# Performance work log

Measured on AMD Instinct MI355X. Metric: run time of the kernel, lower is better.

## Reference

```python
import jax, jax.numpy as jnp
import numpy as np

N_HEAD = 16
N_EMBED = 1024

def setup_inputs() -> dict:
    key = jax.random.key(0)
    ks = jax.random.split(key, 5)
    C = N_EMBED
    x = jax.random.normal(ks[0], (2, 2048, C), dtype=jnp.float32)
    # c_attn: Linear(C, 3C); c_proj: Linear(C, C). PyTorch Linear: y = x @ W.T + b
    w_attn = jax.random.normal(ks[1], (3 * C, C), dtype=jnp.float32) * (1.0 / np.sqrt(C))
    b_attn = jnp.zeros((3 * C,), dtype=jnp.float32)
    w_proj = jax.random.normal(ks[2], (C, C), dtype=jnp.float32) * (1.0 / np.sqrt(C))
    b_proj = jnp.zeros((C,), dtype=jnp.float32)
    return {"x": x, "w_attn": w_attn, "b_attn": b_attn, "w_proj": w_proj, "b_proj": b_proj}

def reference(x, w_attn, b_attn, w_proj, b_proj):
    B, T, C = x.shape
    H = N_HEAD
    D = C // H
    qkv = jnp.einsum('btc,fc->btf', x, w_attn) + b_attn  # [B,T,3C]
    q, k, v = jnp.split(qkv, 3, axis=-1)
    # [B,H,T,D]
    q = q.reshape(B, T, H, D).transpose(0, 2, 1, 3)
    k = k.reshape(B, T, H, D).transpose(0, 2, 1, 3)
    v = v.reshape(B, T, H, D).transpose(0, 2, 1, 3)
    att = jnp.einsum('bhqd,bhkd->bhqk', q, k) * (1.0 / np.sqrt(D))  # [B,H,T,T]
    causal = jnp.tril(jnp.ones((T, T), dtype=bool))
    att = jnp.where(causal[None, None], att, jnp.finfo(att.dtype).min)
    att = jax.nn.softmax(att, axis=-1)
    y = jnp.einsum('bhqk,bhkd->bhqd', att, v)  # [B,H,T,D]
    y = y.transpose(0, 2, 1, 3).reshape(B, T, C)
    return jnp.einsum('btc,fc->btf', y, w_proj) + b_proj
```

## Files before the change

kernel.cpp:

```cpp
#include <hip/hip_runtime.h>
#include <hip/hip_bf16.h>

typedef unsigned short u16;
typedef __attribute__((ext_vector_type(8))) short v8s;
typedef __attribute__((ext_vector_type(4))) short v4s;
typedef __attribute__((ext_vector_type(4))) float v4f;

__device__ __forceinline__ u16 f2bu(float f) {
  union { float f; unsigned u; } v; v.f = f;
  unsigned r = (v.u + 0x7fffu + ((v.u >> 16) & 1u)) >> 16;
  return (u16)r;
}
__device__ __forceinline__ v4s pack4(const v4f& a) {
  union { v4s s; __hip_bfloat162 h[2]; } u;
  u.h[0] = __float22bfloat162_rn(make_float2(a[0], a[1]));
  u.h[1] = __float22bfloat162_rn(make_float2(a[2], a[3]));
  return u.s;
}
__device__ __forceinline__ v8s pack8(const v4f& a, const v4f& b) {
  union { v8s s; __hip_bfloat162 h[4]; } u;
  u.h[0] = __float22bfloat162_rn(make_float2(a[0], a[1]));
  u.h[1] = __float22bfloat162_rn(make_float2(a[2], a[3]));
  u.h[2] = __float22bfloat162_rn(make_float2(b[0], b[1]));
  u.h[3] = __float22bfloat162_rn(make_float2(b[2], b[3]));
  return u.s;
}

__device__ __forceinline__ void g2l16(const u16* g, u16* l) {
  __builtin_amdgcn_global_load_lds((const __attribute__((address_space(1))) void*)g,
                                   (__attribute__((address_space(3))) void*)l,
                                   16, 0, 0);
}

__global__ __launch_bounds__(256) void cvt_bf16(const float* __restrict__ s0, u16* __restrict__ d0, int n0,
                                                const float* __restrict__ s1, u16* __restrict__ d1, int n1,
                                                const float* __restrict__ s2, u16* __restrict__ d2, int n2) {
  int total8 = (n0 + n1 + n2) >> 3;
  for (int i = blockIdx.x * blockDim.x + threadIdx.x; i < total8; i += gridDim.x * blockDim.x) {
    int e = i << 3;
    const float* s; u16* d;
    if (e < n0)            { s = s0 + e;            d = d0 + e; }
    else if (e < n0 + n1)  { s = s1 + (e - n0);     d = d1 + (e - n0); }
    else                   { s = s2 + (e - n0 - n1); d = d2 + (e - n0 - n1); }
    v4f a = *(const v4f*)s, b = *(const v4f*)(s + 4);
    *(v8s*)d = pack8(a, b);
  }
}

__global__ __launch_bounds__(256) void gemm_qkv(const u16* __restrict__ A,
                                                const u16* __restrict__ W,
                                                const float* __restrict__ bias,
                                                u16* __restrict__ o0,
                                                u16* __restrict__ o1,
                                                u16* __restrict__ o2) {
  constexpr int K = 1024;
  __shared__ __align__(16) u16 As[128 * 64];
  __shared__ __align__(16) u16 Bs[128 * 64];
  const int tid = threadIdx.x;
  const int w = tid >> 6, lane = tid & 63, l15 = lane & 15, quad = lane >> 4;
  const int wm = w & 1, wn = w >> 1;
  const int R0 = blockIdx.x * 128, C0 = blockIdx.y * 128;

  v4f acc[4][4] = {};
  const u16* Ag = A + (size_t)R0 * K;
  const u16* Wg = W + (size_t)C0 * K;

  int srow[4], scol[4], sdst[4];
#pragma unroll
  for (int i = 0; i < 4; ++i) {
    int p = (w * 4 + i) * 64 + lane;
    srow[i] = p >> 3;
    scol[i] = (p & 7) * 8;
    sdst[i] = (w * 4 + i) * 512;
  }

  for (int k0 = 0; k0 < K; k0 += 64) {
    if (k0) __syncthreads();
#pragma unroll
    for (int i = 0; i < 4; ++i) g2l16(Ag + srow[i] * K + k0 + scol[i], &As[sdst[i]]);
#pragma unroll
    for (int i = 0; i < 4; ++i) g2l16(Wg + srow[i] * K + k0 + scol[i], &Bs[sdst[i]]);
    __syncthreads();
#pragma unroll
    for (int kk = 0; kk < 2; ++kk) {
      v8s a[4], b[4];
#pragma unroll
      for (int m = 0; m < 4; ++m)
        a[m] = *(const v8s*)&As[(wm * 64 + m * 16 + l15) * 64 + (kk * 4 + quad) * 8];
#pragma unroll
      for (int n = 0; n < 4; ++n)
        b[n] = *(const v8s*)&Bs[(wn * 64 + n * 16 + l15) * 64 + (kk * 4 + quad) * 8];
#pragma unroll
      for (int m = 0; m < 4; ++m)
#pragma unroll
        for (int n = 0; n < 4; ++n)
          acc[m][n] = __builtin_amdgcn_mfma_f32_16x16x32_bf16(a[m], b[n], acc[m][n], 0, 0, 0);
    }
  }

#pragma unroll
  for (int n = 0; n < 4; ++n) {
    int f = C0 + wn * 64 + n * 16 + l15;
    float bv = bias[f];
#pragma unroll
    for (int m = 0; m < 4; ++m) {
      int r0 = R0 + wm * 64 + m * 16 + quad * 4;
      int which = f >> 10, c = f & 1023;
      int h = c >> 6, d = c & 63;
      int b = r0 >> 11, t = r0 & 2047;
      if (which == 2) {
        v4s pk;
#pragma unroll
        for (int reg = 0; reg < 4; ++reg) pk[reg] = (short)f2bu(acc[m][n][reg] + bv);
        *(v4s*)&o2[(((b << 4) + h) * 64 + d) * 2048 + t] = pk;
      } else {
        u16* dst = (which == 0) ? o0 : o1;
#pragma unroll
        for (int reg = 0; reg < 4; ++reg)
          dst[(((b << 4) + h) * 2048 + (t + reg)) * 64 + d] = f2bu(acc[m][n][reg] + bv);
      }
    }
  }
}

__global__ __launch_bounds__(256) void gemm_proj(const u16* __restrict__ A,
                                                 const u16* __restrict__ W,
                                                 const float* __restrict__ bias,
                                                 float* __restrict__ out) {
  constexpr int K = 1024;
  __shared__ __align__(16) u16 As[128 * 64];
  __shared__ __align__(16) u16 Bs[64 * 64];
  const int tid = threadIdx.x;
  const int w = tid >> 6, lane = tid & 63, l15 = lane & 15, quad = lane >> 4;
  const int wm = w & 1, wn = w >> 1;
  const int R0 = blockIdx.x * 128, C0 = blockIdx.y * 64;

  v4f acc[4][2] = {};
  const u16* Ag = A + (size_t)R0 * K;
  const u16* Wg = W + (size_t)C0 * K;

  int arow[4], acol[4], adst[4];
#pragma unroll
  for (int i = 0; i < 4; ++i) {
    int p = (w * 4 + i) * 64 + lane;
    arow[i] = p >> 3; acol[i] = (p & 7) * 8; adst[i] = (w * 4 + i) * 512;
  }
  int brow[2], bcol[2], bdst[2];
#pragma unroll
  for (int i = 0; i < 2; ++i) {
    int p = (w * 2 + i) * 64 + lane;
    brow[i] = p >> 3; bcol[i] = (p & 7) * 8; bdst[i] = (w * 2 + i) * 512;
  }

  for (int k0 = 0; k0 < K; k0 += 64) {
    if (k0) __syncthreads();
#pragma unroll
    for (int i = 0; i < 4; ++i) g2l16(Ag + arow[i] * K + k0 + acol[i], &As[adst[i]]);
#pragma unroll
    for (int i = 0; i < 2; ++i) g2l16(Wg + brow[i] * K + k0 + bcol[i], &Bs[bdst[i]]);
    __syncthreads();
#pragma unroll
    for (int kk = 0; kk < 2; ++kk) {
      v8s a[4], b[2];
#pragma unroll
      for (int m = 0; m < 4; ++m)
        a[m] = *(const v8s*)&As[(wm * 64 + m * 16 + l15) * 64 + (kk * 4 + quad) * 8];
#pragma unroll
      for (int n = 0; n < 2; ++n)
        b[n] = *(const v8s*)&Bs[(wn * 32 + n * 16 + l15) * 64 + (kk * 4 + quad) * 8];
#pragma unroll
      for (int m = 0; m < 4; ++m)
#pragma unroll
        for (int n = 0; n < 2; ++n)
          acc[m][n] = __builtin_amdgcn_mfma_f32_16x16x32_bf16(a[m], b[n], acc[m][n], 0, 0, 0);
    }
  }

#pragma unroll
  for (int n = 0; n < 2; ++n) {
    int f = C0 + wn * 32 + n * 16 + l15;
    float bv = bias[f];
#pragma unroll
    for (int m = 0; m < 4; ++m) {
      int r0 = R0 + wm * 64 + m * 16 + quad * 4;
#pragma unroll
      for (int reg = 0; reg < 4; ++reg)
        out[(size_t)(r0 + reg) * 1024 + f] = acc[m][n][reg] + bv;
    }
  }
}

#define SCL2 0.180336879f
__global__ __launch_bounds__(256, 2) void attn_kernel(const u16* __restrict__ Q,
                                                      const u16* __restrict__ Kt,
                                                      const u16* __restrict__ Vt,
                                                      u16* __restrict__ Y) {
  __shared__ __align__(16) u16 Ksh[2][64 * 64], Vsh[2][64 * 64];
  __shared__ __align__(16) u16 Psh[8 * 16 * 72];
  const int tid = threadIdx.x;
  const int w = tid >> 6, lane = tid & 63, l15 = lane & 15, quad = lane >> 4;
  const int pi = blockIdx.x, h = blockIdx.y, b = blockIdx.z;
  const int qtA = pi, qtB = 31 - pi;
  const int qA0 = qtA * 64, qB0 = qtB * 64;
  const int bh = b * 16 + h;
  const u16* qg = Q + bh * 131072;
  const u16* kg = Kt + bh * 131072;
  const u16* vg = Vt + bh * 131072;

  v8s aqA[2], aqB[2];
  {
    const u16* qrA = qg + (qA0 + w * 16 + l15) * 64;
    const u16* qrB = qg + (qB0 + w * 16 + l15) * 64;
#pragma unroll
    for (int kk = 0; kk < 2; ++kk) {
      aqA[kk] = *(const v8s*)(qrA + kk * 32 + quad * 8);
      aqB[kk] = *(const v8s*)(qrB + kk * 32 + quad * 8);
    }
  }

  v4f OA[4] = {}, OB[4] = {};
  float llA = 0.f, llB = 0.f;
  const int rowlim = w * 16 + l15;

  int srow[2], sgc[2], ssc[2];
  v8s tk[2], tv[2];
#pragma unroll
  for (int i = 0; i < 2; ++i) {
    int cc = (w * 2 + i) * 64 + lane;
    srow[i] = cc >> 3; int c = cc & 7;
    sgc[i] = c * 8; ssc[i] = ((c ^ (srow[i] & 7)) * 8);
    tk[i] = *(const v8s*)(kg + srow[i] * 64 + sgc[i]);
    tv[i] = *(const v8s*)(vg + srow[i] * 2048 + sgc[i]);
  }

  u16* PA = &Psh[(w * 2) * 16 * 72];
  u16* PB = &Psh[(w * 2 + 1) * 16 * 72];

  for (int kt = 0; kt <= qtB; ++kt) {
    const int k0 = kt * 64;
    const int buf = kt & 1;
#pragma unroll
    for (int i = 0; i < 2; ++i) {
      *(v8s*)&Ksh[buf][srow[i] * 64 + ssc[i]] = tk[i];
      *(v8s*)&Vsh[buf][srow[i] * 64 + ssc[i]] = tv[i];
    }
    __syncthreads();
    if (kt < qtB) {
      int kn = k0 + 64;
#pragma unroll
      for (int i = 0; i < 2; ++i) {
        tk[i] = *(const v8s*)(kg + (kn + srow[i]) * 64 + sgc[i]);
        tv[i] = *(const v8s*)(vg + srow[i] * 2048 + kn + sgc[i]);
      }
    }
    const bool doA = (kt <= qtA);
    const u16* Kb = Ksh[buf];
    const u16* Vb = Vsh[buf];

    v4f sA[4], sB[4];
#pragma unroll
    for (int nt = 0; nt < 4; ++nt) {
      v4f zb = {0.f, 0.f, 0.f, 0.f}, za = {0.f, 0.f, 0.f, 0.f};
#pragma unroll
      for (int kk = 0; kk < 2; ++kk) {
        v8s kf = *(const v8s*)&Kb[(nt * 16 + l15) * 64 + (((kk * 4 + quad) ^ (l15 & 7)) * 8)];
        zb = __builtin_amdgcn_mfma_f32_16x16x32_bf16(kf, aqB[kk], zb, 0, 0, 0);
        if (doA) za = __builtin_amdgcn_mfma_f32_16x16x32_bf16(kf, aqA[kk], za, 0, 0, 0);
      }
      sB[nt] = zb; sA[nt] = za;
    }

    {
      float rs = 0.f;
      if (kt == qtB) {
#pragma unroll
        for (int nt = 0; nt < 4; ++nt)
#pragma unroll
          for (int reg = 0; reg < 4; ++reg) {
            int kl = nt * 16 + quad * 4 + reg;
            float p = (kl <= rowlim) ? exp2f(sB[nt][reg] * SCL2) : 0.f;
            sB[nt][reg] = p; rs += p;
          }
      } else {
#pragma unroll
        for (int nt = 0; nt < 4; ++nt)
#pragma unroll
          for (int reg = 0; reg < 4; ++reg) {
            float p = exp2f(sB[nt][reg] * SCL2);
            sB[nt][reg] = p; rs += p;
          }
      }
      llB += rs;
#pragma unroll
      for (int nt = 0; nt < 4; ++nt)
        *(v4s*)&PB[l15 * 72 + nt * 16 + quad * 4] = pack4(sB[nt]);
    }
    if (doA) {
      float rs = 0.f;
      if (kt == qtA) {
#pragma unroll
        for (int nt = 0; nt < 4; ++nt)
#pragma unroll
          for (int reg = 0; reg < 4; ++reg) {
            int kl = nt * 16 + quad * 4 + reg;
            float p = (kl <= rowlim) ? exp2f(sA[nt][reg] * SCL2) : 0.f;
            sA[nt][reg] = p; rs += p;
          }
      } else {
#pragma unroll
        for (int nt = 0; nt < 4; ++nt)
#pragma unroll
          for (int reg = 0; reg < 4; ++reg) {
            float p = exp2f(sA[nt][reg] * SCL2);
            sA[nt][reg] = p; rs += p;
          }
      }
      llA += rs;
#pragma unroll
      for (int nt = 0; nt < 4; ++nt)
        *(v4s*)&PA[l15 * 72 + nt * 16 + quad * 4] = pack4(sA[nt]);
    }

    asm volatile("" ::: "memory");
    v8s apB[2], apA[2];
#pragma unroll
    for (int kk = 0; kk < 2; ++kk) {
      apB[kk] = *(const v8s*)&PB[l15 * 72 + kk * 32 + quad * 8];
      if (doA) apA[kk] = *(const v8s*)&PA[l15 * 72 + kk * 32 + quad * 8];
    }
#pragma unroll
    for (int nt = 0; nt < 4; ++nt)
#pragma unroll
      for (int kk = 0; kk < 2; ++kk) {
        v8s vf = *(const v8s*)&Vb[(nt * 16 + l15) * 64 + (((kk * 4 + quad) ^ (l15 & 7)) * 8)];
        OB[nt] = __builtin_amdgcn_mfma_f32_16x16x32_bf16(apB[kk], vf, OB[nt], 0, 0, 0);
        if (doA) OA[nt] = __builtin_amdgcn_mfma_f32_16x16x32_bf16(apA[kk], vf, OA[nt], 0, 0, 0);
      }
  }

  llB += __shfl_xor(llB, 16, 64); llB += __shfl_xor(llB, 32, 64);
  llA += __shfl_xor(llA, 16, 64); llA += __shfl_xor(llA, 32, 64);
  {
    float li = 1.f / llB, lO[4];
#pragma unroll
    for (int reg = 0; reg < 4; ++reg) lO[reg] = __shfl(li, quad * 4 + reg, 64);
    int tb2 = qB0 + w * 16 + quad * 4;
#pragma unroll
    for (int nt = 0; nt < 4; ++nt)
#pragma unroll
      for (int reg = 0; reg < 4; ++reg)
        Y[(b * 2048 + tb2 + reg) * 1024 + h * 64 + nt * 16 + l15] = f2bu(OB[nt][reg] * lO[reg]);
  }
  {
    float li = 1.f / llA, lO[4];
#pragma unroll
    for (int reg = 0; reg < 4; ++reg) lO[reg] = __shfl(li, quad * 4 + reg, 64);
    int tb2 = qA0 + w * 16 + quad * 4;
#pragma unroll
    for (int nt = 0; nt < 4; ++nt)
#pragma unroll
      for (int reg = 0; reg < 4; ++reg)
        Y[(b * 2048 + tb2 + reg) * 1024 + h * 64 + nt * 16 + l15] = f2bu(OA[nt][reg] * lO[reg]);
  }
}

extern "C" void kernel_launch(void* const* d_in, const int* in_sizes, int n_in,
                              void* d_out, int out_size, void* d_ws, size_t ws_size,
                              hipStream_t stream) {
  const float* x      = (const float*)d_in[0];
  const float* w_attn = (const float*)d_in[1];
  const float* b_attn = (const float*)d_in[2];
  const float* w_proj = (const float*)d_in[3];
  const float* b_proj = (const float*)d_in[4];
  float* out = (float*)d_out;
  char* ws = (char*)d_ws;
  u16* xb  = (u16*)(ws);
  u16* wab = (u16*)(ws + (size_t)( 8u << 20));
  u16* wpb = (u16*)(ws + (size_t)(14u << 20));
  u16* q   = (u16*)(ws + (size_t)(16u << 20));
  u16* k   = (u16*)(ws + (size_t)(24u << 20));
  u16* vt  = (u16*)(ws + (size_t)(32u << 20));
  u16* y   = (u16*)(ws + (size_t)(40u << 20));

  cvt_bf16<<<2048, 256, 0, stream>>>(x, xb, 4194304, w_attn, wab, 3145728, w_proj, wpb, 1048576);
  gemm_qkv<<<dim3(32, 24), 256, 0, stream>>>(xb, wab, b_attn, q, k, vt);
  attn_kernel<<<dim3(16, 16, 2), 256, 0, stream>>>(q, k, vt, y);
  gemm_proj<<<dim3(32, 16), 256, 0, stream>>>(y, wpb, b_proj, out);
}
```

Before: 186.8 us.

## Split attention q-tile pairs across 8 waves and fold softmax scale into Q

The attention kernel now runs 512 threads per block. The paired low and high query tiles are handled by separate groups of 4 waves, so each wave owns a single 16-row strip instead of two. The point is to spread the QK and PV MFMA work across more waves and give better latency hiding. The softmax scale (log2e/sqrt(D)) is also applied to Q in the QKV GEMM epilogue, which removes a multiply per score. The costs are that waves on the low tile sit idle at the barriers once their causal range ends, and the tighter launch bounds (512,4) may cause register pressure or spills.

```diff
diff --git a/kernel.cpp b/kernel.cpp
--- a/kernel.cpp
+++ b/kernel.cpp
@@ -5,6 +5,8 @@
 typedef __attribute__((ext_vector_type(8))) short v8s;
 typedef __attribute__((ext_vector_type(4))) short v4s;
 typedef __attribute__((ext_vector_type(4))) float v4f;
+
+#define SCL2 0.180336879f
 
 __device__ __forceinline__ u16 f2bu(float f) {
   union { float f; unsigned u; } v; v.f = f;
@@ -115,9 +117,10 @@
         *(v4s*)&o2[(((b << 4) + h) * 64 + d) * 2048 + t] = pk;
       } else {
         u16* dst = (which == 0) ? o0 : o1;
+        float sc = (which == 0) ? SCL2 : 1.0f;
 #pragma unroll
         for (int reg = 0; reg < 4; ++reg)
-          dst[(((b << 4) + h) * 2048 + (t + reg)) * 64 + d] = f2bu(acc[m][n][reg] + bv);
+          dst[(((b << 4) + h) * 2048 + (t + reg)) * 64 + d] = f2bu((acc[m][n][reg] + bv) * sc);
       }
     }
   }
@@ -190,8 +193,7 @@
   }
 }
 
-#define SCL2 0.180336879f
-__global__ __launch_bounds__(256, 2) void attn_kernel(const u16* __restrict__ Q,
+__global__ __launch_bounds__(512, 4) void attn_kernel(const u16* __restrict__ Q,
                                                       const u16* __restrict__ Kt,
                                                       const u16* __restrict__ Vt,
                                                       u16* __restrict__ Y) {
@@ -200,168 +202,107 @@
   const int tid = threadIdx.x;
   const int w = tid >> 6, lane = tid & 63, l15 = lane & 15, quad = lane >> 4;
   const int pi = blockIdx.x, h = blockIdx.y, b = blockIdx.z;
-  const int qtA = pi, qtB = 31 - pi;
-  const int qA0 = qtA * 64, qB0 = qtB * 64;
+  const int myqt = (w < 4) ? pi : 31 - pi;
+  const int strip = w & 3;
+  const int q0 = myqt * 64 + strip * 16;
+  const int KT = 32 - pi;
   const int bh = b * 16 + h;
   const u16* qg = Q + bh * 131072;
   const u16* kg = Kt + bh * 131072;
   const u16* vg = Vt + bh * 131072;
 
-  v8s aqA[2], aqB[2];
+  v8s aq[2];
   {
-    const u16* qrA = qg + (qA0 + w * 16 + l15) * 64;
-    const u16* qrB = qg + (qB0 + w * 16 + l15) * 64;
-#pragma unroll
-    for (int kk = 0; kk < 2; ++kk) {
-      aqA[kk] = *(const v8s*)(qrA + kk * 32 + quad * 8);
-      aqB[kk] = *(const v8s*)(qrB + kk * 32 + quad * 8);
-    }
-  }
-
-  v4f OA[4] = {}, OB[4] = {};
-  float llA = 0.f, llB = 0.f;
-  const int rowlim = w * 16 + l15;
-
-  int srow[2], sgc[2], ssc[2];
-  v8s tk[2], tv[2];
-#pragma unroll
-  for (int i = 0; i < 2; ++i) {
-    int cc = (w * 2 + i) * 64 + lane;
-    srow[i] = cc >> 3; int c = cc & 7;
-    sgc[i] = c * 8; ssc[i] = ((c ^ (srow[i] & 7)) * 8);
-    tk[i] = *(const v8s*)(kg + srow[i] * 64 + sgc[i]);
-    tv[i] = *(const v8s*)(vg + srow[i] * 2048 + sgc[i]);
-  }
-
-  u16* PA = &Psh[(w * 2) * 16 * 72];
-  u16* PB = &Psh[(w * 2 + 1) * 16 * 72];
-
-  for (int kt = 0; kt <= qtB; ++kt) {
-    const int k0 = kt * 64;
+    const u16* qr = qg + (q0 + l15) * 64;
+    aq[0] = *(const v8s*)(qr + quad * 8);
+    aq[1] = *(const v8s*)(qr + 32 + quad * 8);
+  }
+
+  v4f O[4] = {};
+  float ll = 0.f;
+  const int rowlim = strip * 16 + l15;
+
+  const int srow = tid >> 3, cc = tid & 7;
+  const int sgc = cc * 8, ssc = (cc ^ (srow & 7)) * 8;
+  v8s tk = *(const v8s*)(kg + srow * 64 + sgc);
+  v8s tv = *(const v8s*)(vg + srow * 2048 + sgc);
+
+  u16* Pw = &Psh[w * 16 * 72];
+
+  for (int kt = 0; kt < KT; ++kt) {
     const int buf = kt & 1;
-#pragma unroll
-    for (int i = 0; i < 2; ++i) {
-      *(v8s*)&Ksh[buf][srow[i] * 64 + ssc[i]] = tk[i];
-      *(v8s*)&Vsh[buf][srow[i] * 64 + ssc[i]] = tv[i];
-    }
+    *(v8s*)&Ksh[buf][srow * 64 + ssc] = tk;
+    *(v8s*)&Vsh[buf][srow * 64 + ssc] = tv;
     __syncthreads();
-    if (kt < qtB) {
-      int kn = k0 + 64;
-#pragma unroll
-      for (int i = 0; i < 2; ++i) {
-        tk[i] = *(const v8s*)(kg + (kn + srow[i]) * 64 + sgc[i]);
-        tv[i] = *(const v8s*)(vg + srow[i] * 2048 + kn + sgc[i]);
+    if (kt + 1 < KT) {
+      int kn = (kt + 1) * 64;
+      tk = *(const v8s*)(kg + (kn + srow) * 64 + sgc);
+      tv = *(const v8s*)(vg + srow * 2048 + kn + sgc);
+    }
+    if (kt <= myqt) {
+      const u16* Kb = Ksh[buf];
+      const u16* Vb = Vsh[buf];
+
+      v4f s[4];
+#pragma unroll
+      for (int nt = 0; nt < 4; ++nt) {
+        v4f z = {0.f, 0.f, 0.f, 0.f};
+#pragma unroll
+        for (int kk = 0; kk < 2; ++kk) {
+          v8s kf = *(const v8s*)&Kb[(nt * 16 + l15) * 64 + (((kk * 4 + quad) ^ (l15 & 7)) * 8)];
+          z = __builtin_amdgcn_mfma_f32_16x16x32_bf16(kf, aq[kk], z, 0, 0, 0);
+        }
+        s[nt] = z;
       }
-    }
-    const bool doA = (kt <= qtA);
-    const u16* Kb = Ksh[buf];
-    const u16* Vb = Vsh[buf];
-
-    v4f sA[4], sB[4];
-#pragma unroll
-    for (int nt = 0; nt < 4; ++nt) {
-      v4f zb = {0.f, 0.f, 0.f, 0.f}, za = {0.f, 0.f, 0.f, 0.f};
-#pragma unroll
-      for (int kk = 0; kk < 2; ++kk) {
-        v8s kf = *(const v8s*)&Kb[(nt * 16 + l15) * 64 + (((kk * 4 + quad) ^ (l15 & 7)) * 8)];
-        zb = __builtin_amdgcn_mfma_f32_16x16x32_bf16(kf, aqB[kk], zb, 0, 0, 0);
-        if (doA) za = __builtin_amdgcn_mfma_f32_16x16x32_bf16(kf, aqA[kk], za, 0, 0, 0);
-      }
-      sB[nt] = zb; sA[nt] = za;
-    }
-
-    {
+
       float rs = 0.f;
-      if (kt == qtB) {
+      if (kt == myqt) {
 #pragma unroll
         for (int nt = 0; nt < 4; ++nt)
 #pragma unroll
           for (int reg = 0; reg < 4; ++reg) {
             int kl = nt * 16 + quad * 4 + reg;
-            float p = (kl <= rowlim) ? exp2f(sB[nt][reg] * SCL2) : 0.f;
-            sB[nt][reg] = p; rs += p;
+            float p = (kl <= rowlim) ? exp2f(s[nt][reg]) : 0.f;
+            s[nt][reg] = p; rs += p;
           }
       } else {
 #pragma unroll
         for (int nt = 0; nt < 4; ++nt)
 #pragma unroll
           for (int reg = 0; reg < 4; ++reg) {
-            float p = exp2f(sB[nt][reg] * SCL2);
-            sB[nt][reg] = p; rs += p;
+            float p = exp2f(s[nt][reg]);
+            s[nt][reg] = p; rs += p;
           }
       }
-      llB += rs;
+      ll += rs;
 #pragma unroll
       for (int nt = 0; nt < 4; ++nt)
-        *(v4s*)&PB[l15 * 72 + nt * 16 + quad * 4] = pack4(sB[nt]);
-    }
-    if (doA) {
-      float rs = 0.f;
-      if (kt == qtA) {
-#pragma unroll
-        for (int nt = 0; nt < 4; ++nt)
-#pragma unroll
-          for (int reg = 0; reg < 4; ++reg) {
-            int kl = nt * 16 + quad * 4 + reg;
-            float p = (kl <= rowlim) ? exp2f(sA[nt][reg] * SCL2) : 0.f;
-            sA[nt][reg] = p; rs += p;
-          }
-      } else {
-#pragma unroll
-        for (int nt = 0; nt < 4; ++nt)
-#pragma unroll
-          for (int reg = 0; reg < 4; ++reg) {
-            float p = exp2f(sA[nt][reg] * SCL2);
-            sA[nt][reg] = p; rs += p;
-          }
-      }
-      llA += rs;
+        *(v4s*)&Pw[l15 * 72 + nt * 16 + quad * 4] = pack4(s[nt]);
+
+      asm volatile("" ::: "memory");
+      v8s ap[2];
+      ap[0] = *(const v8s*)&Pw[l15 * 72 + quad * 8];
+      ap[1] = *(const v8s*)&Pw[l15 * 72 + 32 + quad * 8];
 #pragma unroll
       for (int nt = 0; nt < 4; ++nt)
-        *(v4s*)&PA[l15 * 72 + nt * 16 + quad * 4] = pack4(sA[nt]);
-    }
-
-    asm volatile("" ::: "memory");
-    v8s apB[2], apA[2];
-#pragma unroll
-    for (int kk = 0; kk < 2; ++kk) {
-      apB[kk] = *(const v8s*)&PB[l15 * 72 + kk * 32 + quad * 8];
-      if (doA) apA[kk] = *(const v8s*)&PA[l15 * 72 + kk * 32 + quad * 8];
-    }
-#pragma unroll
-    for (int nt = 0; nt < 4; ++nt)
-#pragma unroll
-      for (int kk = 0; kk < 2; ++kk) {
-        v8s vf = *(const v8s*)&Vb[(nt * 16 + l15) * 64 + (((kk * 4 + quad) ^ (l15 & 7)) * 8)];
-        OB[nt] = __builtin_amdgcn_mfma_f32_16x16x32_bf16(apB[kk], vf, OB[nt], 0, 0, 0);
-        if (doA) OA[nt] = __builtin_amdgcn_mfma_f32_16x16x32_bf16(apA[kk], vf, OA[nt], 0, 0, 0);
-      }
-  }
-
-  llB += __shfl_xor(llB, 16, 64); llB += __shfl_xor(llB, 32, 64);
-  llA += __shfl_xor(llA, 16, 64); llA += __shfl_xor(llA, 32, 64);
-  {
-    float li = 1.f / llB, lO[4];
-#pragma unroll
-    for (int reg = 0; reg < 4; ++reg) lO[reg] = __shfl(li, quad * 4 + reg, 64);
-    int tb2 = qB0 + w * 16 + quad * 4;
-#pragma unroll
-    for (int nt = 0; nt < 4; ++nt)
-#pragma unroll
-      for (int reg = 0; reg < 4; ++reg)
-        Y[(b * 2048 + tb2 + reg) * 1024 + h * 64 + nt * 16 + l15] = f2bu(OB[nt][reg] * lO[reg]);
-  }
-  {
-    float li = 1.f / llA, lO[4];
-#pragma unroll
-    for (int reg = 0; reg < 4; ++reg) lO[reg] = __shfl(li, quad * 4 + reg, 64);
-    int tb2 = qA0 + w * 16 + quad * 4;
-#pragma unroll
-    for (int nt = 0; nt < 4; ++nt)
-#pragma unroll
-      for (int reg = 0; reg < 4; ++reg)
-        Y[(b * 2048 + tb2 + reg) * 1024 + h * 64 + nt * 16 + l15] = f2bu(OA[nt][reg] * lO[reg]);
-  }
+#pragma unroll
+        for (int kk = 0; kk < 2; ++kk) {
+          v8s vf = *(const v8s*)&Vb[(nt * 16 + l15) * 64 + (((kk * 4 + quad) ^ (l15 & 7)) * 8)];
+          O[nt] = __builtin_amdgcn_mfma_f32_16x16x32_bf16(ap[kk], vf, O[nt], 0, 0, 0);
+        }
+    }
+  }
+
+  ll += __shfl_xor(ll, 16, 64); ll += __shfl_xor(ll, 32, 64);
+  float li = 1.f / ll, lO[4];
+#pragma unroll
+  for (int reg = 0; reg < 4; ++reg) lO[reg] = __shfl(li, quad * 4 + reg, 64);
+  const int tb = q0 + quad * 4;
+#pragma unroll
+  for (int nt = 0; nt < 4; ++nt)
+#pragma unroll
+    for (int reg = 0; reg < 4; ++reg)
+      Y[(b * 2048 + tb + reg) * 1024 + h * 64 + nt * 16 + l15] = f2bu(O[nt][reg] * lO[reg]);
 }
 
 extern "C" void kernel_launch(void* const* d_in, const int* in_sizes, int n_in,
@@ -384,6 +325,6 @@
 
   cvt_bf16<<<2048, 256, 0, stream>>>(x, xb, 4194304, w_attn, wab, 3145728, w_proj, wpb, 1048576);
   gemm_qkv<<<dim3(32, 24), 256, 0, stream>>>(xb, wab, b_attn, q, k, vt);
-  attn_kernel<<<dim3(16, 16, 2), 256, 0, stream>>>(q, k, vt, y);
+  attn_kernel<<<dim3(16, 16, 2), 512, 0, stream>>>(q, k, vt, y);
   gemm_proj<<<dim3(32, 16), 256, 0, stream>>>(y, wpb, b_proj, out);
 }
```

Measured after the change: 174.1 us. 1.07x faster.
